# Kernel optimization log

Measured on AMD Instinct MI355X. Metric: run time of the kernel, lower is better.

## Reference

```python
import jax, jax.numpy as jnp
from jax import lax
import numpy as np

DIM = 256


def setup_inputs() -> dict:
    key = jax.random.key(0)
    ks = jax.random.split(key, 7)
    B, C, H, W = 16, DIM, 64, 64
    s = 0.02
    return {
        "x": jax.random.normal(ks[0], (B, C, H, W), dtype=jnp.float32),
        "qkv_w": jax.random.normal(ks[1], (3 * C, C), dtype=jnp.float32) * s,
        "qkv_b": jnp.zeros((3 * C,), dtype=jnp.float32),
        "proj_w": jax.random.normal(ks[2], (C, C), dtype=jnp.float32) * s,
        "proj_b": jnp.zeros((C,), dtype=jnp.float32),
        "conv_w": jax.random.normal(ks[3], (C, C, 3, 3), dtype=jnp.float32) * s,
        "conv_b": jnp.zeros((C,), dtype=jnp.float32),
    }


def reference(x, qkv_w, qkv_b, proj_w, proj_b, conv_w, conv_b):
    B, C, H, W = x.shape
    N = H * W
    scale = C ** (-0.5)
    # qkv on channels-last tokens: [B,N,3C]
    xp = x.transpose(0, 2, 3, 1).reshape(B, N, C)
    qkv = xp @ qkv_w.T + qkv_b
    q, k, v = jnp.split(qkv, 3, axis=-1)  # each [B,N,C]
    q = q.transpose(0, 2, 1)  # [B,C,N]
    v = v.transpose(0, 2, 1)  # [B,C,N]
    # channel attention: [B,C,C]
    attn = jax.nn.softmax(jnp.einsum('bcn,bnd->bcd', q, k) * scale, axis=-1)
    out = jnp.einsum('bcd,bdn->bcn', attn, v).transpose(0, 2, 1)  # [B,N,C]
    out = out @ proj_w.T + proj_b  # [B,N,C]
    # faithful to original: direct reshape [B,N,C] -> [B,C,H,W]
    attn_out = out.reshape(B, C, H, W)
    conv_out = lax.conv_general_dilated(
        x, conv_w, window_strides=(1, 1), padding=[(1, 1), (1, 1)],
        dimension_numbers=('NCHW', 'OIHW', 'NCHW'))
    conv_out = conv_out + conv_b[None, :, None, None]
    return attn_out + conv_out
```

## Files before the change

kernel.cpp:

```cpp
#include <hip/hip_runtime.h>
#include <hip/hip_bf16.h>

typedef unsigned short u16;
typedef __bf16 bf16x8 __attribute__((ext_vector_type(8)));
typedef float f32x4 __attribute__((ext_vector_type(4)));

#define BATCH 16
#define C 256
#define NTOK 4096
#define CN 1048576

__device__ __forceinline__ u16 f2b(float f) {
  __hip_bfloat16 h = __float2bfloat16(f);
  return __builtin_bit_cast(u16, h);
}
__device__ __forceinline__ float b2f(u16 u) {
  unsigned int x = ((unsigned int)u) << 16;
  return __builtin_bit_cast(float, x);
}

__device__ __forceinline__ void glds16(const u16* g, u16* l) {
  __builtin_amdgcn_global_load_lds(
      (const __attribute__((address_space(1))) unsigned int*)(g),
      (__attribute__((address_space(3))) unsigned int*)(l), 16, 0, 0);
}

__global__ __launch_bounds__(256) void prep_x_kernel(
    const float* __restrict__ x, u16* __restrict__ xbf, u16* __restrict__ xT,
    float* __restrict__ rws) {
  __shared__ float t[32][33];
  int b = blockIdx.z;
  int c0 = blockIdx.y * 32, n0 = blockIdx.x * 32;
  int tid = threadIdx.x;
  int i = tid >> 3, j4 = (tid & 7) * 4;
  const float* xb = x + (long)b * CN;
  float4 v = *(const float4*)(xb + (long)(c0 + i) * NTOK + n0 + j4);
  ushort4 bv;
  bv.x = f2b(v.x); bv.y = f2b(v.y); bv.z = f2b(v.z); bv.w = f2b(v.w);
  *(ushort4*)(xbf + (long)b * CN + (long)(c0 + i) * NTOK + n0 + j4) = bv;
  t[i][j4 + 0] = v.x; t[i][j4 + 1] = v.y; t[i][j4 + 2] = v.z; t[i][j4 + 3] = v.w;
  __syncthreads();
  ushort4 o;
  o.x = f2b(t[j4 + 0][i]); o.y = f2b(t[j4 + 1][i]);
  o.z = f2b(t[j4 + 2][i]); o.w = f2b(t[j4 + 3][i]);
  *(ushort4*)(xT + (long)b * CN + (long)(n0 + i) * C + c0 + j4) = o;
  if (tid < 32) {
    float s = 0.f;
#pragma unroll
    for (int j = 0; j < 32; ++j) s += t[tid][j];
    atomicAdd(&rws[b * C + c0 + tid], s);
  }
}

__global__ __launch_bounds__(256) void prep_w_kernel(
    const float* __restrict__ qkv_w, const float* __restrict__ proj_w,
    const float* __restrict__ conv_w, u16* __restrict__ WqT, u16* __restrict__ Wk,
    u16* __restrict__ WvT, u16* __restrict__ Pw, u16* __restrict__ cw,
    float* __restrict__ rws, u16* __restrict__ zbuf) {
  int idx = blockIdx.x * 256 + threadIdx.x;
  if (idx < 4096) rws[idx] = 0.f;
  if (idx < 256) zbuf[idx] = 0;
  if (idx < 65536) {
    WqT[(idx & 255) * 256 + (idx >> 8)] = f2b(qkv_w[idx]);
  } else if (idx < 131072) {
    int e = idx - 65536;
    Wk[e] = f2b(qkv_w[65536 + e]);
  } else if (idx < 196608) {
    int e = idx - 131072;
    int i = e >> 8, d = e & 255;
    WvT[e] = f2b(qkv_w[131072 + d * 256 + i]);
  } else if (idx < 262144) {
    int e = idx - 196608;
    Pw[e] = f2b(proj_w[e]);
  } else if (idx < 851968) {
    int e = idx - 262144;
    int o = e / 2304;
    int rem = e - o * 2304;
    int tap = rem >> 8, i = rem & 255;
    cw[e] = f2b(conv_w[o * 2304 + i * 9 + tap]);
  }
}

template <int EPI>
__global__ __launch_bounds__(256, 2) void gemm_glds_kernel(
    const u16* __restrict__ A, const u16* __restrict__ B, void* __restrict__ Cv,
    int K, int lda, int ldb, int ldc, int tilesN, long sA, long sB, long sC,
    float scale, const float* __restrict__ e1, const float* __restrict__ e2,
    const float* __restrict__ e3, const float* __restrict__ e4, int e34stride) {
  if (EPI == 4 && blockIdx.x == 4) {
    int bb = blockIdx.z, j = threadIdx.x;
    const u16* m = A + (long)bb * sA + (long)j * 256;
    float s = 0.f;
    for (int d = 0; d < 256; ++d) s += b2f(m[d]) * e1[512 + d];
    float* cbout = const_cast<float*>(e4);
    cbout[bb * 256 + j] = e2[j] + s;
    return;
  }
  int b = blockIdx.z, ks = blockIdx.y;
  A += (long)b * sA + (long)ks * K;
  B += (long)b * sB + (long)ks * K;
  int ty = blockIdx.x / tilesN, tx = blockIdx.x % tilesN;
  int row0 = ty * 128, col0 = tx * 128;

  __shared__ u16 lA[2][4096];
  __shared__ u16 lB[2][4096];

  int tid = threadIdx.x;
  int lane = tid & 63, wv = tid >> 6;
  int wm = wv >> 1, wn = wv & 1;
  int fr = lane & 15, kq = lane >> 4;
  int kqs = kq ^ ((fr >> 1) & 3);

  int c0 = wv * 128 + lane, c1 = c0 + 64;
  int r0s = c0 >> 2, r1s = c1 >> 2;
  int ls0 = (c0 & 3) ^ ((r0s >> 1) & 3);
  int ls1 = (c1 & 3) ^ ((r1s >> 1) & 3);
  const u16* pA0 = A + (long)(row0 + r0s) * lda + ls0 * 8;
  const u16* pA1 = A + (long)(row0 + r1s) * lda + ls1 * 8;
  const u16* pB0 = B + (long)(col0 + r0s) * ldb + ls0 * 8;
  const u16* pB1 = B + (long)(col0 + r1s) * ldb + ls1 * 8;
  int dst0 = wv * 1024, dst1 = wv * 1024 + 512;

  f32x4 acc[4][4] = {};

  auto STAGE = [&](int buf, int t) {
    int k0 = t << 5;
    glds16(pA0 + k0, &lA[buf][dst0]);
    glds16(pA1 + k0, &lA[buf][dst1]);
    glds16(pB0 + k0, &lB[buf][dst0]);
    glds16(pB1 + k0, &lB[buf][dst1]);
  };
  auto COMPUTE = [&](int buf) {
    bf16x8 af[4], bfr[4];
#pragma unroll
    for (int m = 0; m < 4; ++m)
      af[m] = *(const bf16x8*)&lA[buf][(wm * 64 + m * 16 + fr) * 32 + kqs * 8];
#pragma unroll
    for (int n = 0; n < 4; ++n)
      bfr[n] = *(const bf16x8*)&lB[buf][(wn * 64 + n * 16 + fr) * 32 + kqs * 8];
#pragma unroll
    for (int m = 0; m < 4; ++m)
#pragma unroll
      for (int n = 0; n < 4; ++n)
        acc[m][n] = __builtin_amdgcn_mfma_f32_16x16x32_bf16(af[m], bfr[n], acc[m][n], 0, 0, 0);
  };

  int nk = K >> 5, cur = 0;
  STAGE(0, 0);
  __syncthreads();
  for (int t = 0; t < nk; ++t) {
    if (t + 1 < nk) STAGE(cur ^ 1, t + 1);
    COMPUTE(cur);
    __syncthreads();
    cur ^= 1;
  }

  if (EPI == 0) {
    float* Cb = (float*)Cv + ((long)b * 4 + ks) * sC;
#pragma unroll
    for (int m = 0; m < 4; ++m)
#pragma unroll
      for (int n = 0; n < 4; ++n)
#pragma unroll
        for (int r = 0; r < 4; ++r) {
          int gr = row0 + wm * 64 + m * 16 + kq * 4 + r;
          int gc = col0 + wn * 64 + n * 16 + fr;
          Cb[(long)gr * ldc + gc] = acc[m][n][r];
        }
  } else if (EPI == 1 || EPI == 4) {
    __hip_bfloat16* Cb = (__hip_bfloat16*)Cv + (long)b * sC;
#pragma unroll
    for (int m = 0; m < 4; ++m)
#pragma unroll
      for (int n = 0; n < 4; ++n)
#pragma unroll
        for (int r = 0; r < 4; ++r) {
          int gr = row0 + wm * 64 + m * 16 + kq * 4 + r;
          int gc = col0 + wn * 64 + n * 16 + fr;
          Cb[(long)gr * ldc + gc] = __float2bfloat16(acc[m][n][r]);
        }
  } else if (EPI == 2) {
    float* Cb = (float*)Cv + (long)b * sC;
    const float* ub = e3 + (long)b * e34stride;
    const float* wb = e4 + (long)b * e34stride;
#pragma unroll
    for (int m = 0; m < 4; ++m)
#pragma unroll
      for (int n = 0; n < 4; ++n)
#pragma unroll
        for (int r = 0; r < 4; ++r) {
          int gr = row0 + wm * 64 + m * 16 + kq * 4 + r;
          int gc = col0 + wn * 64 + n * 16 + fr;
          float v = acc[m][n][r] + e1[gr] * ub[gc] + e2[gc] * wb[gr] +
                    4096.0f * e1[gr] * e2[gc];
          Cb[(long)gr * ldc + gc] = v * scale;
        }
  }
}

__global__ __launch_bounds__(256) void reduceG_T1_bias_kernel(
    const float* __restrict__ Gp, const u16* __restrict__ WqT,
    u16* __restrict__ T1, const float* __restrict__ qkv_w,
    const float* __restrict__ r, float* __restrict__ u, float* __restrict__ w) {
  int b = blockIdx.y;
  if (blockIdx.x < 64) {
    __shared__ float g[4][256];
    int tid = threadIdx.x;
    int e = blockIdx.x * 1024 + tid * 4;
    const float* base = Gp + (long)b * 262144;
    float4 s = *(const float4*)(base + e);
#pragma unroll
    for (int sl = 1; sl < 4; ++sl) {
      float4 v = *(const float4*)(base + sl * 65536 + e);
      s.x += v.x; s.y += v.y; s.z += v.z; s.w += v.w;
    }
    int rr = tid >> 6, cc = (tid & 63) * 4;
    g[rr][cc + 0] = s.x; g[rr][cc + 1] = s.y;
    g[rr][cc + 2] = s.z; g[rr][cc + 3] = s.w;
    __syncthreads();
    int c = tid;
    float a0 = 0.f, a1 = 0.f, a2 = 0.f, a3 = 0.f;
#pragma unroll 4
    for (int i = 0; i < 256; ++i) {
      float wq = b2f(WqT[i * 256 + c]);
      a0 += wq * g[0][i]; a1 += wq * g[1][i];
      a2 += wq * g[2][i]; a3 += wq * g[3][i];
    }
    ushort4 o;
    o.x = f2b(a0); o.y = f2b(a1); o.z = f2b(a2); o.w = f2b(a3);
    *(ushort4*)(T1 + (long)b * 65536 + (long)c * 256 + blockIdx.x * 4) = o;
  } else {
    int t = threadIdx.x;
    const float* rb = r + b * C;
    float su = 0.f, sw = 0.f;
    for (int i = 0; i < C; ++i) {
      float rv = rb[i];
      su += qkv_w[(256 + t) * 256 + i] * rv;
      sw += qkv_w[t * 256 + i] * rv;
    }
    u[b * C + t] = su;
    w[b * C + t] = sw;
  }
}

__global__ __launch_bounds__(256) void softmax_kernel(const float* __restrict__ S,
                                                      u16* __restrict__ attnT) {
  int row = blockIdx.x;
  int t = threadIdx.x;
  float v = S[(long)row * C + t];
  __shared__ float red[256];
  red[t] = v; __syncthreads();
  for (int st = 128; st > 0; st >>= 1) {
    if (t < st) red[t] = fmaxf(red[t], red[t + st]);
    __syncthreads();
  }
  float mx = red[0];
  __syncthreads();
  float e = __expf(v - mx);
  red[t] = e; __syncthreads();
  for (int st = 128; st > 0; st >>= 1) {
    if (t < st) red[t] += red[t + st];
    __syncthreads();
  }
  float inv = 1.0f / red[0];
  int b = row >> 8, c = row & 255;
  attnT[(long)b * 65536 + t * 256 + c] = f2b(e * inv);
}

__global__ __launch_bounds__(256, 2) void convattn_kernel(
    const u16* __restrict__ xT, const u16* __restrict__ cw,
    const u16* __restrict__ W2, const u16* __restrict__ zbuf,
    const float* __restrict__ conv_b, const float* __restrict__ cb,
    float* __restrict__ out) {
  int b = blockIdx.y;
  int to = blockIdx.x >> 5;
  int tn = blockIdx.x & 31;
  int row0 = to * 128, col0 = tn * 128;
  const u16* xTb = xT + (long)b * CN;
  const u16* W2b = W2 + (long)b * 65536;

  __shared__ u16 lA[2][4096];
  __shared__ u16 lB[2][4096];

  int tid = threadIdx.x;
  int lane = tid & 63, wv = tid >> 6;
  int wm = wv >> 1, wn = wv & 1;
  int fr = lane & 15, kq = lane >> 4;
  int kqs = kq ^ ((fr >> 1) & 3);

  int c0 = wv * 128 + lane, c1 = c0 + 64;
  int r0s = c0 >> 2, r1s = c1 >> 2;
  int ls0 = (c0 & 3) ^ ((r0s >> 1) & 3);
  int ls1 = (c1 & 3) ^ ((r1s >> 1) & 3);
  int dst0 = wv * 1024, dst1 = wv * 1024 + 512;

  const u16* pA0 = cw + (long)(row0 + r0s) * 2304 + ls0 * 8;
  const u16* pA1 = cw + (long)(row0 + r1s) * 2304 + ls1 * 8;
  int t0 = col0 + r0s, t1 = col0 + r1s;
  int h0 = t0 >> 6, w0_ = t0 & 63, h1 = t1 >> 6, w1_ = t1 & 63;
  const u16* pB0 = xTb + (long)t0 * 256 + ls0 * 8;
  const u16* pB1 = xTb + (long)t1 * 256 + ls1 * 8;
  const u16* zs0 = zbuf + ls0 * 8;
  const u16* zs1 = zbuf + ls1 * 8;
  int nb = col0 >> 8, jb = col0 & 255;
  const u16* qA0 = xTb + (long)((row0 + r0s) * 16 + nb) * 256 + ls0 * 8;
  const u16* qA1 = xTb + (long)((row0 + r1s) * 16 + nb) * 256 + ls1 * 8;
  const u16* qB0 = W2b + (long)(jb + r0s) * 256 + ls0 * 8;
  const u16* qB1 = W2b + (long)(jb + r1s) * 256 + ls1 * 8;

  f32x4 acc[4][4] = {};
  const u16 *at0, *at1, *bt0, *bt1;

  auto set_tap = [&](int tap) {
    int dh = tap / 3 - 1, dw = tap % 3 - 1;
    long sh = (long)(dh * 64 + dw) * 256;
    at0 = pA0 + tap * 256;
    at1 = pA1 + tap * 256;
    bool v0 = ((unsigned)(h0 + dh) < 64u) && ((unsigned)(w0_ + dw) < 64u);
    bool v1 = ((unsigned)(h1 + dh) < 64u) && ((unsigned)(w1_ + dw) < 64u);
    bt0 = v0 ? pB0 + sh : zs0;
    bt1 = v1 ? pB1 + sh : zs1;
  };
  auto set_attn = [&]() {
    at0 = qA0; at1 = qA1; bt0 = qB0; bt1 = qB1;
  };

  auto STAGE = [&](int buf, int chunk) {
    int k0 = chunk << 5;
    glds16(at0 + k0, &lA[buf][dst0]);
    glds16(at1 + k0, &lA[buf][dst1]);
    glds16(bt0 + k0, &lB[buf][dst0]);
    glds16(bt1 + k0, &lB[buf][dst1]);
  };
  auto COMPUTE = [&](int buf) {
    bf16x8 af[4], bfr[4];
#pragma unroll
    for (int m = 0; m < 4; ++m)
      af[m] = *(const bf16x8*)&lA[buf][(wm * 64 + m * 16 + fr) * 32 + kqs * 8];
#pragma unroll
    for (int n = 0; n < 4; ++n)
      bfr[n] = *(const bf16x8*)&lB[buf][(wn * 64 + n * 16 + fr) * 32 + kqs * 8];
    __builtin_amdgcn_s_setprio(1);
#pragma unroll
    for (int m = 0; m < 4; ++m)
#pragma unroll
      for (int n = 0; n < 4; ++n)
        acc[m][n] = __builtin_amdgcn_mfma_f32_16x16x32_bf16(af[m], bfr[n], acc[m][n], 0, 0, 0);
    __builtin_amdgcn_s_setprio(0);
  };

  set_tap(0);
  STAGE(0, 0);
  asm volatile("s_waitcnt vmcnt(0)" ::: "memory");
  __builtin_amdgcn_sched_barrier(0);
  __builtin_amdgcn_s_barrier();
  __builtin_amdgcn_sched_barrier(0);

  int buf = 0;
#pragma unroll 1
  for (int T = 0; T < 10; ++T) {
#pragma unroll
    for (int j = 0; j < 8; ++j) {
      if (!(T == 9 && j == 7)) {
        if (j == 7) {
          if (T < 8) set_tap(T + 1);
          else set_attn();
          STAGE(buf ^ 1, 0);
        } else {
          STAGE(buf ^ 1, j + 1);
        }
      }
      COMPUTE(buf);
      asm volatile("s_waitcnt vmcnt(0)" ::: "memory");
      __builtin_amdgcn_sched_barrier(0);
      __builtin_amdgcn_s_barrier();
      __builtin_amdgcn_sched_barrier(0);
      buf ^= 1;
    }
  }

  float* ob = out + (long)b * CN;
  const float* cbb = cb + b * C;
#pragma unroll
  for (int m = 0; m < 4; ++m) {
    int go = row0 + wm * 64 + m * 16 + kq * 4;
#pragma unroll
    for (int nn = 0; nn < 4; ++nn) {
      int cc = wn * 64 + nn * 16 + fr;
      float cbv = cbb[jb + cc];
#pragma unroll
      for (int r = 0; r < 4; ++r)
        ob[(long)(go + r) * NTOK + col0 + cc] =
            acc[m][nn][r] + conv_b[go + r] + cbv;
    }
  }
}

extern "C" void kernel_launch(void* const* d_in, const int* in_sizes, int n_in,
                              void* d_out, int out_size, void* d_ws, size_t ws_size,
                              hipStream_t stream) {
  const float* x = (const float*)d_in[0];
  const float* qkv_w = (const float*)d_in[1];
  const float* qkv_b = (const float*)d_in[2];
  const float* proj_w = (const float*)d_in[3];
  const float* proj_b = (const float*)d_in[4];
  const float* conv_w = (const float*)d_in[5];
  const float* conv_b = (const float*)d_in[6];
  float* out = (float*)d_out;
  char* ws = (char*)d_ws;

  u16* xbf = (u16*)(ws);
  u16* xT = (u16*)(ws + 33554432);
  u16* T1bf = (u16*)(ws + 67108864);
  float* Gpart = (float*)(ws + 69206016);
  float* Sf = (float*)(ws + 71303168);
  u16* attnT = (u16*)(ws + 75497472);
  u16* Mbf = (u16*)(ws + 77594624);
  u16* W2bf = (u16*)(ws + 79691776);
  u16* WqT = (u16*)(ws + 85983232);
  u16* Wk = (u16*)(ws + 86114304);
  u16* WvT = (u16*)(ws + 86245376);
  u16* Pw = (u16*)(ws + 86376448);
  u16* cw = (u16*)(ws + 86507520);
  float* rws = (float*)(ws + 87687168);
  float* uws = (float*)(ws + 87703552);
  float* wws = (float*)(ws + 87719936);
  float* cb = (float*)(ws + 87736320);
  u16* zbuf = (u16*)(ws + 87752704);

  prep_w_kernel<<<3328, 256, 0, stream>>>(qkv_w, proj_w, conv_w, WqT, Wk, WvT,
                                          Pw, cw, rws, zbuf);
  prep_x_kernel<<<dim3(128, 8, BATCH), 256, 0, stream>>>(x, xbf, xT, rws);

  gemm_glds_kernel<0><<<dim3(4, 4, BATCH), 256, 0, stream>>>(
      xbf, xbf, Gpart, 1024, 4096, 4096, 256, 2, CN, CN, 65536,
      0.f, nullptr, nullptr, nullptr, nullptr, 0);
  reduceG_T1_bias_kernel<<<dim3(65, BATCH), 256, 0, stream>>>(
      Gpart, WqT, T1bf, qkv_w, rws, uws, wws);

  gemm_glds_kernel<2><<<dim3(4, 1, BATCH), 256, 0, stream>>>(
      T1bf, Wk, Sf, 256, 256, 256, 256, 2, 65536, 0, 65536,
      0.0625f, qkv_b, qkv_b + 256, uws, wws, 256);

  softmax_kernel<<<BATCH * C, 256, 0, stream>>>(Sf, attnT);

  gemm_glds_kernel<1><<<dim3(4, 1, BATCH), 256, 0, stream>>>(
      Pw, attnT, Mbf, 256, 256, 256, 256, 2, 0, 65536, 65536,
      0.f, nullptr, nullptr, nullptr, nullptr, 0);
  gemm_glds_kernel<4><<<dim3(5, 1, BATCH), 256, 0, stream>>>(
      Mbf, WvT, W2bf, 256, 256, 256, 256, 2, 65536, 0, 65536,
      0.f, qkv_b, proj_b, nullptr, cb, 256);

  convattn_kernel<<<dim3(64, BATCH), 256, 0, stream>>>(xT, cw, W2bf, zbuf,
                                                       conv_b, cb, out);
}
```

Before: 231.6 us.

## Enlarge conv-attention GEMM tile to 128x256 per block

The fused conv+attention output kernel now computes a 128x256 output tile per block instead of 128x128, with each wave holding 4x8 MFMA accumulators. The loader mapping is reorganized so each wave stages two A rows-groups and four B row-groups. The aim is more MFMA work per LDS load and less A-operand refetch. The cost is higher register and LDS use and only 512 blocks, which may reduce occupancy and wave-level parallelism on a large-CU GPU.

```diff
diff --git a/kernel.cpp b/kernel.cpp
--- a/kernel.cpp
+++ b/kernel.cpp
@@ -273,78 +273,85 @@
     const float* __restrict__ conv_b, const float* __restrict__ cb,
     float* __restrict__ out) {
   int b = blockIdx.y;
-  int to = blockIdx.x >> 5;
-  int tn = blockIdx.x & 31;
-  int row0 = to * 128, col0 = tn * 128;
+  int to = blockIdx.x >> 4;
+  int tn = blockIdx.x & 15;
+  int row0 = to * 128, col0 = tn * 256;
   const u16* xTb = xT + (long)b * CN;
   const u16* W2b = W2 + (long)b * 65536;
 
   __shared__ u16 lA[2][4096];
-  __shared__ u16 lB[2][4096];
+  __shared__ u16 lB[2][8192];
 
   int tid = threadIdx.x;
-  int lane = tid & 63, wv = tid >> 6;
-  int wm = wv >> 1, wn = wv & 1;
+  int lane = tid & 63, w = tid >> 6;
+  int wm = w >> 1, wn = w & 1;
   int fr = lane & 15, kq = lane >> 4;
   int kqs = kq ^ ((fr >> 1) & 3);
 
-  int c0 = wv * 128 + lane, c1 = c0 + 64;
-  int r0s = c0 >> 2, r1s = c1 >> 2;
-  int ls0 = (c0 & 3) ^ ((r0s >> 1) & 3);
-  int ls1 = (c1 & 3) ^ ((r1s >> 1) & 3);
-  int dst0 = wv * 1024, dst1 = wv * 1024 + 512;
-
-  const u16* pA0 = cw + (long)(row0 + r0s) * 2304 + ls0 * 8;
-  const u16* pA1 = cw + (long)(row0 + r1s) * 2304 + ls1 * 8;
-  int t0 = col0 + r0s, t1 = col0 + r1s;
-  int h0 = t0 >> 6, w0_ = t0 & 63, h1 = t1 >> 6, w1_ = t1 & 63;
-  const u16* pB0 = xTb + (long)t0 * 256 + ls0 * 8;
-  const u16* pB1 = xTb + (long)t1 * 256 + ls1 * 8;
-  const u16* zs0 = zbuf + ls0 * 8;
-  const u16* zs1 = zbuf + ls1 * 8;
-  int nb = col0 >> 8, jb = col0 & 255;
-  const u16* qA0 = xTb + (long)((row0 + r0s) * 16 + nb) * 256 + ls0 * 8;
-  const u16* qA1 = xTb + (long)((row0 + r1s) * 16 + nb) * 256 + ls1 * 8;
-  const u16* qB0 = W2b + (long)(jb + r0s) * 256 + ls0 * 8;
-  const u16* qB1 = W2b + (long)(jb + r1s) * 256 + ls1 * 8;
-
-  f32x4 acc[4][4] = {};
-  const u16 *at0, *at1, *bt0, *bt1;
+  int lr = lane >> 2;
+  int ls = (lane & 3) ^ ((lane >> 3) & 3);
+
+  const u16* pA[2];
+#pragma unroll
+  for (int i = 0; i < 2; ++i)
+    pA[i] = cw + (long)(row0 + w * 32 + i * 16 + lr) * 2304 + ls * 8;
+  const u16* pB[4]; int hh[4], ww[4];
+#pragma unroll
+  for (int i = 0; i < 4; ++i) {
+    int t = col0 + w * 64 + i * 16 + lr;
+    hh[i] = t >> 6; ww[i] = t & 63;
+    pB[i] = xTb + (long)t * 256 + ls * 8;
+  }
+  const u16* zsrc = zbuf + ls * 8;
+
+  f32x4 acc[4][8] = {};
+  const u16 *at0, *at1, *bt0, *bt1, *bt2, *bt3;
 
   auto set_tap = [&](int tap) {
     int dh = tap / 3 - 1, dw = tap % 3 - 1;
     long sh = (long)(dh * 64 + dw) * 256;
-    at0 = pA0 + tap * 256;
-    at1 = pA1 + tap * 256;
-    bool v0 = ((unsigned)(h0 + dh) < 64u) && ((unsigned)(w0_ + dw) < 64u);
-    bool v1 = ((unsigned)(h1 + dh) < 64u) && ((unsigned)(w1_ + dw) < 64u);
-    bt0 = v0 ? pB0 + sh : zs0;
-    bt1 = v1 ? pB1 + sh : zs1;
+    at0 = pA[0] + tap * 256;
+    at1 = pA[1] + tap * 256;
+    bool v0 = ((unsigned)(hh[0] + dh) < 64u) && ((unsigned)(ww[0] + dw) < 64u);
+    bool v1 = ((unsigned)(hh[1] + dh) < 64u) && ((unsigned)(ww[1] + dw) < 64u);
+    bool v2 = ((unsigned)(hh[2] + dh) < 64u) && ((unsigned)(ww[2] + dw) < 64u);
+    bool v3 = ((unsigned)(hh[3] + dh) < 64u) && ((unsigned)(ww[3] + dw) < 64u);
+    bt0 = v0 ? pB[0] + sh : zsrc;
+    bt1 = v1 ? pB[1] + sh : zsrc;
+    bt2 = v2 ? pB[2] + sh : zsrc;
+    bt3 = v3 ? pB[3] + sh : zsrc;
   };
   auto set_attn = [&]() {
-    at0 = qA0; at1 = qA1; bt0 = qB0; bt1 = qB1;
+    at0 = xTb + (long)((row0 + w * 32 + 0 + lr) * 16 + tn) * 256 + ls * 8;
+    at1 = xTb + (long)((row0 + w * 32 + 16 + lr) * 16 + tn) * 256 + ls * 8;
+    bt0 = W2b + (long)(w * 64 + 0 + lr) * 256 + ls * 8;
+    bt1 = W2b + (long)(w * 64 + 16 + lr) * 256 + ls * 8;
+    bt2 = W2b + (long)(w * 64 + 32 + lr) * 256 + ls * 8;
+    bt3 = W2b + (long)(w * 64 + 48 + lr) * 256 + ls * 8;
   };
 
   auto STAGE = [&](int buf, int chunk) {
     int k0 = chunk << 5;
-    glds16(at0 + k0, &lA[buf][dst0]);
-    glds16(at1 + k0, &lA[buf][dst1]);
-    glds16(bt0 + k0, &lB[buf][dst0]);
-    glds16(bt1 + k0, &lB[buf][dst1]);
+    glds16(at0 + k0, &lA[buf][(w * 32 + 0) * 32]);
+    glds16(at1 + k0, &lA[buf][(w * 32 + 16) * 32]);
+    glds16(bt0 + k0, &lB[buf][(w * 64 + 0) * 32]);
+    glds16(bt1 + k0, &lB[buf][(w * 64 + 16) * 32]);
+    glds16(bt2 + k0, &lB[buf][(w * 64 + 32) * 32]);
+    glds16(bt3 + k0, &lB[buf][(w * 64 + 48) * 32]);
   };
   auto COMPUTE = [&](int buf) {
-    bf16x8 af[4], bfr[4];
+    bf16x8 af[4], bfr[8];
 #pragma unroll
     for (int m = 0; m < 4; ++m)
       af[m] = *(const bf16x8*)&lA[buf][(wm * 64 + m * 16 + fr) * 32 + kqs * 8];
 #pragma unroll
-    for (int n = 0; n < 4; ++n)
-      bfr[n] = *(const bf16x8*)&lB[buf][(wn * 64 + n * 16 + fr) * 32 + kqs * 8];
+    for (int n = 0; n < 8; ++n)
+      bfr[n] = *(const bf16x8*)&lB[buf][(wn * 128 + n * 16 + fr) * 32 + kqs * 8];
     __builtin_amdgcn_s_setprio(1);
 #pragma unroll
     for (int m = 0; m < 4; ++m)
 #pragma unroll
-      for (int n = 0; n < 4; ++n)
+      for (int n = 0; n < 8; ++n)
         acc[m][n] = __builtin_amdgcn_mfma_f32_16x16x32_bf16(af[m], bfr[n], acc[m][n], 0, 0, 0);
     __builtin_amdgcn_s_setprio(0);
   };
@@ -385,9 +392,9 @@
   for (int m = 0; m < 4; ++m) {
     int go = row0 + wm * 64 + m * 16 + kq * 4;
 #pragma unroll
-    for (int nn = 0; nn < 4; ++nn) {
-      int cc = wn * 64 + nn * 16 + fr;
-      float cbv = cbb[jb + cc];
+    for (int nn = 0; nn < 8; ++nn) {
+      int cc = wn * 128 + nn * 16 + fr;
+      float cbv = cbb[cc];
 #pragma unroll
       for (int r = 0; r < 4; ++r)
         ob[(long)(go + r) * NTOK + col0 + cc] =
@@ -451,6 +458,6 @@
       Mbf, WvT, W2bf, 256, 256, 256, 256, 2, 65536, 0, 65536,
       0.f, qkv_b, proj_b, nullptr, cb, 256);
 
-  convattn_kernel<<<dim3(64, BATCH), 256, 0, stream>>>(xT, cw, W2bf, zbuf,
+  convattn_kernel<<<dim3(32, BATCH), 256, 0, stream>>>(xT, cw, W2bf, zbuf,
                                                        conv_b, cb, out);
 }
```

Result: slower. 302.9 us (+30.8%).
